# Performance work log

Measured on AMD Instinct MI355X. Metric: run time of the kernel, lower is better.

Reference implementation:

```python
import jax, jax.numpy as jnp
import numpy as np

SCORE_THR = 0.05
IOU_THR = 0.5
TOPK = 1000  # per-class candidate cap (static shape for jit)


def _make_anchors(img):
    """RetinaNet anchors: 9 per location over P3-P7 (strides 8..128)."""
    strides = [8, 16, 32, 64, 128]
    sizes = [32, 64, 128, 256, 512]
    ratios = [0.5, 1.0, 2.0]
    scales = [2.0 ** 0, 2.0 ** (1.0 / 3.0), 2.0 ** (2.0 / 3.0)]
    out = []
    for stride, size in zip(strides, sizes):
        ws, hs = [], []
        for r in ratios:
            for sc in scales:
                a = (size * sc) ** 2
                w = np.sqrt(a / r)
                ws.append(w)
                hs.append(w * r)
        ws = np.asarray(ws)
        hs = np.asarray(hs)
        fs = img // stride
        c = (np.arange(fs) + 0.5) * stride
        cy, cx = np.meshgrid(c, c, indexing='ij')
        cx = cx.reshape(-1)[:, None]
        cy = cy.reshape(-1)[:, None]
        boxes = np.stack([cx - ws / 2, cy - hs / 2, cx + ws / 2, cy + hs / 2], axis=-1)
        out.append(boxes.reshape(-1, 4))
    return np.concatenate(out, axis=0).astype(np.float32)


def setup_inputs() -> dict:
    key = jax.random.key(0)
    k1, k2 = jax.random.split(key)
    img = 1024
    anchors = jnp.asarray(_make_anchors(img))          # [196416, 4]
    A = anchors.shape[0]
    cls_heads = jax.random.uniform(k1, (1, A, 80), dtype=jnp.float32)   # post-sigmoid probs
    reg_heads = jax.random.normal(k2, (1, A, 4), dtype=jnp.float32)
    return {"cls_heads": cls_heads, "reg_heads": reg_heads, "anchors": anchors,
            "img_h": img, "img_w": img}


def _decode(anchors, deltas):
    # BBoxTransform: std = [0.1, 0.1, 0.2, 0.2]
    w = anchors[:, 2] - anchors[:, 0]
    h = anchors[:, 3] - anchors[:, 1]
    cx = anchors[:, 0] + 0.5 * w
    cy = anchors[:, 1] + 0.5 * h
    dx = deltas[:, 0] * 0.1
    dy = deltas[:, 1] * 0.1
    dw = deltas[:, 2] * 0.2
    dh = deltas[:, 3] * 0.2
    pcx = cx + dx * w
    pcy = cy + dy * h
    pw = jnp.exp(dw) * w
    ph = jnp.exp(dh) * h
    return jnp.stack([pcx - 0.5 * pw, pcy - 0.5 * ph,
                      pcx + 0.5 * pw, pcy + 0.5 * ph], axis=-1)


def _iou(b):  # [K,4] -> [K,K]
    area = jnp.maximum(b[:, 2] - b[:, 0], 0) * jnp.maximum(b[:, 3] - b[:, 1], 0)
    lt = jnp.maximum(b[:, None, :2], b[None, :, :2])
    rb = jnp.minimum(b[:, None, 2:], b[None, :, 2:])
    wh = jnp.maximum(rb - lt, 0.0)
    inter = wh[..., 0] * wh[..., 1]
    union = area[:, None] + area[None, :] - inter
    return inter / jnp.maximum(union, 1e-8)


def _nms_one_class(scores_c, boxes):
    # threshold, take top-K candidates (static shape), greedy NMS
    masked = jnp.where(scores_c > SCORE_THR, scores_c, -1.0)
    _, idx = jax.lax.top_k(masked, TOPK)
    s = scores_c[idx]                       # [K]
    b = boxes[idx]                          # [K,4]
    valid = s > SCORE_THR
    iou = _iou(b)                           # [K,K]
    rng = jnp.arange(TOPK)

    def body(i, keep):
        sup = (iou[i] > IOU_THR) & (rng > i) & keep[i]
        return keep & ~sup

    keep = jax.lax.fori_loop(0, TOPK, body, valid)
    return jnp.where(keep, s, 0.0), jnp.where(keep[:, None], b, 0.0), keep


def reference(cls_heads, reg_heads, anchors, img_h, img_w):
    # batch = 1 (the torch code squeezes the batch dim)
    scores_ac = cls_heads[0]                # [A, C]
    deltas = reg_heads[0]                   # [A, 4]
    boxes = _decode(anchors, deltas)        # [A, 4]
    # ClipBoxes
    boxes = jnp.stack([
        jnp.clip(boxes[:, 0], 0.0, img_w),
        jnp.clip(boxes[:, 1], 0.0, img_h),
        jnp.clip(boxes[:, 2], 0.0, img_w),
        jnp.clip(boxes[:, 3], 0.0, img_h)], axis=-1)
    scores_ca = scores_ac.T                 # [C, A]
    s, b, keep = jax.vmap(_nms_one_class, in_axes=(0, None))(scores_ca, boxes)
    C = scores_ca.shape[0]
    cls_idx = jnp.where(keep, jnp.arange(C)[:, None], -1)
    # padded, static-shape equivalent of (finalScores, finalAnchorBoxesIndexes,
    # finalAnchorBoxesCoordinates); invalid slots have score 0 / class -1
    return s.reshape(-1), cls_idx.reshape(-1), b.reshape(-1, 4)
```

## Files before the change

kernel.cpp:

```cpp
#include <hip/hip_runtime.h>
#include <hip/hip_bf16.h>
#include <math.h>

typedef unsigned long long u64;
typedef unsigned int u32;

#define C_NUM 80
#define TOPK 1000
#define CAP 2048
#define HB 128
#define STG 32
#define NCHUNK 16
#define SCORE_THR 0.05f
#define IOU_THR 0.5f
#define GRID_SCAN 256

__device__ __forceinline__ float exp_cr(float x) {
    return (float)exp((double)x);
}

__device__ __forceinline__ void decode_box(const float* __restrict__ anch,
                                           const float* __restrict__ reg,
                                           int a, float fw, float fh, float4* out) {
#pragma clang fp contract(off)
    float a0 = anch[(size_t)a * 4 + 0], a1 = anch[(size_t)a * 4 + 1];
    float a2 = anch[(size_t)a * 4 + 2], a3 = anch[(size_t)a * 4 + 3];
    float d0 = reg[(size_t)a * 4 + 0], d1 = reg[(size_t)a * 4 + 1];
    float d2 = reg[(size_t)a * 4 + 2], d3 = reg[(size_t)a * 4 + 3];
    float w = a2 - a0, h = a3 - a1;
    float cx = a0 + 0.5f * w, cy = a1 + 0.5f * h;
    float dx = d0 * 0.1f, dy = d1 * 0.1f, dw = d2 * 0.2f, dh = d3 * 0.2f;
    float t1 = dx * w; float pcx = cx + t1;
    float t2 = dy * h; float pcy = cy + t2;
    float pw = exp_cr(dw) * w;
    float ph = exp_cr(dh) * h;
    float x1 = pcx - 0.5f * pw, y1 = pcy - 0.5f * ph;
    float x2 = pcx + 0.5f * pw, y2 = pcy + 0.5f * ph;
    x1 = fminf(fmaxf(x1, 0.0f), fw);
    y1 = fminf(fmaxf(y1, 0.0f), fh);
    x2 = fminf(fmaxf(x2, 0.0f), fw);
    y2 = fminf(fmaxf(y2, 0.0f), fh);
    *out = make_float4(x1, y1, x2, y2);
}

__global__ __launch_bounds__(1024)
void hist_kernel(const float4* __restrict__ cls4, u32* __restrict__ slices,
                 u32* __restrict__ cntG, int nvec) {
    __shared__ u32 h[C_NUM * HB];
    int tid = threadIdx.x;
    if (blockIdx.x == 0 && tid < C_NUM) cntG[tid] = 0u;
    for (int i = tid; i < C_NUM * HB; i += 1024) h[i] = 0u;
    __syncthreads();
    int gid = blockIdx.x * 1024 + tid;
    const int stride = GRID_SCAN * 1024;
    const int dC = (stride * 4) % C_NUM;
    int c0 = (gid * 4) % C_NUM;
    for (int v = gid; v < nvec; v += stride) {
        float4 f = cls4[v];
        float e[4] = {f.x, f.y, f.z, f.w};
        int cc = c0;
#pragma unroll
        for (int k = 0; k < 4; ++k) {
            int t = (((int)__float_as_uint(e[k])) - 0x3F000000) >> 16;
            if (t > 0) {
                t = t > HB - 1 ? HB - 1 : t;
                atomicAdd(&h[cc * HB + t], 1u);
            }
            cc++; if (cc == C_NUM) cc = 0;
        }
        c0 += dC; if (c0 >= C_NUM) c0 -= C_NUM;
    }
    __syncthreads();
    u32* my = slices + (size_t)blockIdx.x * (C_NUM * HB);
    for (int i = tid; i < C_NUM * HB; i += 1024) my[i] = h[i];
}

__global__ __launch_bounds__(1024)
void thr_kernel(const u32* __restrict__ slices, u32* __restrict__ thrG) {
    __shared__ u32 part[8][HB];
    __shared__ u32 s[HB];
    __shared__ int bsel;
    int c = blockIdx.x, tid = threadIdx.x;
    int b = tid & (HB - 1), g = tid >> 7;
    u32 sum = 0;
    const u32* base = slices + c * HB + b;
    for (int sl = g * 32; sl < g * 32 + 32; ++sl)
        sum += base[(size_t)sl * (C_NUM * HB)];
    part[g][b] = sum;
    if (tid == 0) bsel = 0;
    __syncthreads();
    if (tid < HB) {
        u32 t = 0;
#pragma unroll
        for (int g2 = 0; g2 < 8; ++g2) t += part[g2][tid];
        s[tid] = t;
    }
    __syncthreads();
    for (int d = 1; d < HB; d <<= 1) {
        u32 v = 0;
        if (tid < HB) v = s[tid] + ((tid + d < HB) ? s[tid + d] : 0u);
        __syncthreads();
        if (tid < HB) s[tid] = v;
        __syncthreads();
    }
    if (tid < HB) {
        u32 me = s[tid];
        u32 nxt = (tid < HB - 1) ? s[tid + 1] : 0u;
        if (me >= (u32)TOPK && (tid == HB - 1 || nxt < (u32)TOPK)) bsel = tid;
    }
    __syncthreads();
    if (tid == 0) {
        int bb = bsel;
        thrG[c] = (bb == 0) ? 0u : (u32)(0x3F000000 + (bb << 16));
    }
}

__global__ __launch_bounds__(1024)
void gather_kernel(const float4* __restrict__ cls4, const u32* __restrict__ thrG,
                   u32* __restrict__ cntG, u64* __restrict__ pool, int nvec) {
    __shared__ int thrS[C_NUM];
    __shared__ u32 lcnt[C_NUM];
    __shared__ u32 lbase[C_NUM];
    __shared__ u64 stage[C_NUM * STG];
    int tid = threadIdx.x;
    if (tid < C_NUM) { thrS[tid] = (int)thrG[tid]; lcnt[tid] = 0u; }
    __syncthreads();

    int gid = blockIdx.x * 1024 + tid;
    const int stride = GRID_SCAN * 1024;
    const int dA = (stride * 4) / C_NUM;
    const int dC = (stride * 4) % C_NUM;
    int base = gid * 4;
    int aa0 = base / C_NUM;
    int c0 = base - aa0 * C_NUM;
    for (int v = gid; v < nvec; v += stride) {
        float4 f = cls4[v];
        float e[4] = {f.x, f.y, f.z, f.w};
        int cc = c0, aa = aa0;
#pragma unroll
        for (int k = 0; k < 4; ++k) {
            int bits = (int)__float_as_uint(e[k]);
            if (bits >= thrS[cc]) {
                u64 key = ((u64)(u32)bits << 32) | (u64)(u32)(~(u32)aa);
                u32 p = atomicAdd(&lcnt[cc], 1u);
                if (p < STG) stage[cc * STG + p] = key;
                else {
                    u32 q = atomicAdd(&cntG[cc], 1u);
                    if (q < CAP) pool[(size_t)cc * CAP + q] = key;
                }
            }
            cc++; if (cc == C_NUM) { cc = 0; aa++; }
        }
        c0 += dC;
        if (c0 >= C_NUM) { c0 -= C_NUM; aa0 += dA + 1; } else aa0 += dA;
    }
    __syncthreads();
    if (tid < C_NUM) {
        u32 nl = lcnt[tid]; if (nl > STG) nl = STG;
        lbase[tid] = nl ? atomicAdd(&cntG[tid], nl) : 0u;
        lcnt[tid] = nl;
    }
    __syncthreads();
    for (int i = tid; i < C_NUM * STG; i += 1024) {
        int c = i >> 5, k = i & (STG - 1);
        if ((u32)k < lcnt[c]) {
            u32 q = lbase[c] + (u32)k;
            if (q < CAP) pool[(size_t)c * CAP + q] = stage[i];
        }
    }
}

__global__ __launch_bounds__(256)
void rank_kernel(const u64* __restrict__ pool, const u32* __restrict__ cntG,
                 const float* __restrict__ anchors, const float* __restrict__ regs,
                 const int* __restrict__ imh, const int* __restrict__ imw,
                 u64* __restrict__ sortedKey, float4* __restrict__ candBox,
                 float* __restrict__ candArea) {
    __shared__ __align__(16) u64 keys[CAP];
    int c = blockIdx.x, q = blockIdx.y, tid = threadIdx.x;
    int n = (int)cntG[c]; if (n > CAP) n = CAP;
    int my = q * 256 + tid;
    if (my >= n && my < TOPK) {
        int g = c * TOPK + my;
        sortedKey[g] = 0ull;
        candBox[g] = make_float4(0.f, 0.f, 0.f, 0.f);
        candArea[g] = 0.f;
    }
    if (q * 256 >= n) return;
    for (int i = tid; i < n; i += 256) keys[i] = pool[(size_t)c * CAP + i];
    __syncthreads();
    u64 k0 = (my < n) ? keys[my] : ~0ull;
    int r0 = 0;
    int j = 0;
    for (; j + 8 <= n; j += 8) {
        ulonglong2 p0 = *(const ulonglong2*)&keys[j];
        ulonglong2 p1 = *(const ulonglong2*)&keys[j + 2];
        ulonglong2 p2 = *(const ulonglong2*)&keys[j + 4];
        ulonglong2 p3 = *(const ulonglong2*)&keys[j + 6];
        r0 += (int)(p0.x > k0) + (int)(p0.y > k0)
            + (int)(p1.x > k0) + (int)(p1.y > k0)
            + (int)(p2.x > k0) + (int)(p2.y > k0)
            + (int)(p3.x > k0) + (int)(p3.y > k0);
    }
    for (; j < n; ++j) r0 += (int)(keys[j] > k0);
    if (my < n && r0 < TOPK) {
        float sc = __uint_as_float((u32)(k0 >> 32));
        int a = (int)(~(u32)k0);
        float fw = (float)(*imw), fh = (float)(*imh);
        float4 bx = make_float4(0.f, 0.f, 0.f, 0.f);
        if (sc > SCORE_THR) decode_box(anchors, regs, a, fw, fh, &bx);
        int g = c * TOPK + r0;
        sortedKey[g] = k0;
        candBox[g] = bx;
        candArea[g] = fmaxf(bx.z - bx.x, 0.0f) * fmaxf(bx.w - bx.y, 0.0f);
    }
}

__global__ __launch_bounds__(512)
void iou_kernel(const float4* __restrict__ candBox, const float* __restrict__ candArea,
                u64* __restrict__ supT) {
#pragma clang fp contract(off)
    __shared__ float4 box[NCHUNK * 64];
    __shared__ float area[NCHUNK * 64];
    int c = blockIdx.x, bq = blockIdx.y;
    int tid = threadIdx.x, lane = tid & 63, wave = tid >> 6;
    for (int i = tid; i < NCHUNK * 64; i += 512) {
        if (i < TOPK) {
            box[i] = candBox[(size_t)c * TOPK + i];
            area[i] = candArea[(size_t)c * TOPK + i];
        } else {
            box[i] = make_float4(0.f, 0.f, 0.f, 0.f);
            area[i] = 0.f;
        }
    }
    __syncthreads();

    int wid = bq * 8 + wave;
    int q = 0, rem = wid;
    while (rem >= ((17 - q) >> 1)) { rem -= (17 - q) >> 1; ++q; }
    int jwA = q + 2 * rem;
    int jwB = jwA + 1;
    bool hasB = (jwB < NCHUNK);
    bool diag = (rem == 0);

    int rowBase = q << 6;
    int jA = (jwA << 6) | lane;
    int jB = hasB ? ((jwB << 6) | lane) : jA;
    float4 bjA = box[jA]; float ajA = area[jA];
    float4 bjB = box[jB]; float ajB = area[jB];
    u64 vwA = 0ull, vwB = 0ull;

#pragma unroll 16
    for (int r = 0; r < 64; ++r) {
        int i = rowBase + r;
        float4 bi = box[i];
        float ai = area[i];
        float ltxA = fmaxf(bi.x, bjA.x), ltyA = fmaxf(bi.y, bjA.y);
        float rbxA = fminf(bi.z, bjA.z), rbyA = fminf(bi.w, bjA.w);
        float wwA = fmaxf(rbxA - ltxA, 0.0f), hhA = fmaxf(rbyA - ltyA, 0.0f);
        float interA = wwA * hhA;
        float dA = fmaxf((ai + ajA) - interA, 1e-8f);
        bool supA = (interA + interA) > dA;
        float ltxB = fmaxf(bi.x, bjB.x), ltyB = fmaxf(bi.y, bjB.y);
        float rbxB = fminf(bi.z, bjB.z), rbyB = fminf(bi.w, bjB.w);
        float wwB = fmaxf(rbxB - ltxB, 0.0f), hhB = fmaxf(rbyB - ltyB, 0.0f);
        float interB = wwB * hhB;
        float dB = fmaxf((ai + ajB) - interB, 1e-8f);
        bool supB = (interB + interB) > dB;

        u64 wA = __ballot(supA);
        u64 wB = __ballot(supB);
        if (diag) wA &= (((~0ull) << 1) << r);
        bool sel = (lane == r);
        vwA = sel ? wA : vwA;
        vwB = sel ? wB : vwB;
    }

    int rowEnd = TOPK - rowBase; if (rowEnd > 64) rowEnd = 64;
    u64* clsBase = supT + (size_t)c * (NCHUNK * 1024);
    if (lane < rowEnd) {
        clsBase[(size_t)jwA * 1024 + rowBase + lane] = vwA;
        if (hasB) clsBase[(size_t)jwB * 1024 + rowBase + lane] = vwB;
    }
}

__global__ __launch_bounds__(1024)
void nmsout_kernel(const u64* __restrict__ supT, const u64* __restrict__ sortedKey,
                   const float4* __restrict__ candBox, float* __restrict__ out) {
    __shared__ __align__(16) u64 supLds[NCHUNK * 1024];
    __shared__ u64 km[NCHUNK];
    __shared__ u64 maskArr[NCHUNK * 64];
    __shared__ int changed;
    int c = blockIdx.x, tid = threadIdx.x;
    int lane = tid & 63, wave = tid >> 6;

    const u64* base = supT + (size_t)c * (NCHUNK * 1024);
#pragma unroll
    for (int jw = 0; jw < NCHUNK; ++jw) {
        int R = (jw + 1) << 6; if (R > TOPK) R = TOPK;
        for (int i = tid; i < R; i += 1024)
            supLds[jw * 1024 + i] = base[(size_t)jw * 1024 + i];
    }

    u64 key = (tid < TOPK) ? sortedKey[c * TOPK + tid] : 0ull;
    float sc = __uint_as_float((u32)(key >> 32));
    bool valid = (tid < TOPK) && (sc > SCORE_THR);
    u64 kwValid = __ballot(valid);
    if (lane == 0) km[wave] = kwValid;
    if (tid == 0) changed = 1;
    __syncthreads();

    while (changed) {
        maskArr[tid] = 0ull - ((km[wave] >> lane) & 1ull);
        __syncthreads();
        if (tid == 0) changed = 0;
        u64 acc = 0ull;
        int R = (wave + 1) << 6;
        for (int i = lane; i < R; i += 64)
            acc |= supLds[wave * 1024 + i] & maskArr[i];
        u32 lo = (u32)acc, hi = (u32)(acc >> 32);
#pragma unroll
        for (int s = 1; s < 64; s <<= 1) {
            lo |= __shfl_xor(lo, s);
            hi |= __shfl_xor(hi, s);
        }
        u64 nk = kwValid & ~(((u64)hi << 32) | lo);
        __syncthreads();
        if (lane == 0) {
            if (nk != km[wave]) changed = 1;
            km[wave] = nk;
        }
        __syncthreads();
    }

    u64 kw = km[wave];
    if (tid < TOPK) {
        bool keep = (kw >> lane) & 1ull;
        int g = c * TOPK + tid;
        out[g] = keep ? sc : 0.0f;
        out[C_NUM * TOPK + g] = keep ? (float)c : -1.0f;
        float4 b = keep ? candBox[(size_t)c * TOPK + tid]
                        : make_float4(0.f, 0.f, 0.f, 0.f);
        ((float4*)(out + 2 * C_NUM * TOPK))[g] = b;
    }
}

extern "C" void kernel_launch(void* const* d_in, const int* in_sizes, int n_in,
                              void* d_out, int out_size, void* d_ws, size_t ws_size,
                              hipStream_t stream) {
    const float* cls  = (const float*)d_in[0];
    const float* reg  = (const float*)d_in[1];
    const float* anch = (const float*)d_in[2];
    const int* imh    = (const int*)d_in[3];
    const int* imw    = (const int*)d_in[4];
    int A = in_sizes[2] / 4;
    int nvec = (A * C_NUM) / 4;

    char* w = (char*)d_ws;
    size_t off = 0;
    auto alloc = [&](size_t bytes) -> void* {
        off = (off + 255) & ~(size_t)255;
        void* p = w + off;
        off += bytes;
        return p;
    };
    u32*    cntG      = (u32*)   alloc((size_t)C_NUM * 4);
    u32*    thrG      = (u32*)   alloc((size_t)C_NUM * 4);
    u32*    slices    = (u32*)   alloc((size_t)GRID_SCAN * C_NUM * HB * 4);
    u64*    pool      = (u64*)   alloc((size_t)C_NUM * CAP * 8);
    u64*    sortedKey = (u64*)   alloc((size_t)C_NUM * TOPK * 8);
    float4* candBox   = (float4*)alloc((size_t)C_NUM * TOPK * 16);
    float*  candArea  = (float*) alloc((size_t)C_NUM * TOPK * 4);
    u64*    supT      = (u64*)   alloc((size_t)C_NUM * NCHUNK * 1024 * 8);

    hist_kernel<<<GRID_SCAN, 1024, 0, stream>>>((const float4*)cls, slices, cntG, nvec);
    thr_kernel<<<C_NUM, 1024, 0, stream>>>(slices, thrG);
    gather_kernel<<<GRID_SCAN, 1024, 0, stream>>>((const float4*)cls, thrG, cntG, pool, nvec);
    rank_kernel<<<dim3(C_NUM, 8), 256, 0, stream>>>(pool, cntG, anch, reg, imh, imw,
                                                    sortedKey, candBox, candArea);
    iou_kernel<<<dim3(C_NUM, 9), 512, 0, stream>>>(candBox, candArea, supT);
    nmsout_kernel<<<C_NUM, 1024, 0, stream>>>(supT, sortedKey, candBox, (float*)d_out);
}
```

Before: 107.1 us.

## Build IoU bitmasks per lane with shift-or instead of ballots; simplify NMS mask loop

The IoU kernel now gives each lane one row box and loops over the 64 column boxes (read as LDS broadcasts), building each suppression word with a shift-or. This replaces the two ballots and lane-select per row, and the diagonal mask is applied once at the end. Blocks shrink to 256 threads and the grid doubles to keep the same wave count. The NMS loop drops the shared maskArr and its extra barrier, reading keep bits straight from km, and each thread's candidate box is loaded before the loop instead of at output time.

```diff
diff --git a/kernel.cpp b/kernel.cpp
--- a/kernel.cpp
+++ b/kernel.cpp
@@ -216,7 +216,7 @@
     }
 }
 
-__global__ __launch_bounds__(512)
+__global__ __launch_bounds__(256)
 void iou_kernel(const float4* __restrict__ candBox, const float* __restrict__ candArea,
                 u64* __restrict__ supT) {
 #pragma clang fp contract(off)
@@ -224,7 +224,7 @@
     __shared__ float area[NCHUNK * 64];
     int c = blockIdx.x, bq = blockIdx.y;
     int tid = threadIdx.x, lane = tid & 63, wave = tid >> 6;
-    for (int i = tid; i < NCHUNK * 64; i += 512) {
+    for (int i = tid; i < NCHUNK * 64; i += 256) {
         if (i < TOPK) {
             box[i] = candBox[(size_t)c * TOPK + i];
             area[i] = candArea[(size_t)c * TOPK + i];
@@ -235,47 +235,44 @@
     }
     __syncthreads();
 
-    int wid = bq * 8 + wave;
+    int wid = bq * 4 + wave;
     int q = 0, rem = wid;
     while (rem >= ((17 - q) >> 1)) { rem -= (17 - q) >> 1; ++q; }
     int jwA = q + 2 * rem;
     int jwB = jwA + 1;
     bool hasB = (jwB < NCHUNK);
-    bool diag = (rem == 0);
 
     int rowBase = q << 6;
-    int jA = (jwA << 6) | lane;
-    int jB = hasB ? ((jwB << 6) | lane) : jA;
-    float4 bjA = box[jA]; float ajA = area[jA];
-    float4 bjB = box[jB]; float ajB = area[jB];
+    int i = rowBase + lane;
+    float4 bi = box[i];
+    float ai = area[i];
+    int jbA = jwA << 6;
+    int jbB = hasB ? (jwB << 6) : jbA;
     u64 vwA = 0ull, vwB = 0ull;
 
 #pragma unroll 16
-    for (int r = 0; r < 64; ++r) {
-        int i = rowBase + r;
-        float4 bi = box[i];
-        float ai = area[i];
+    for (int jj = 63; jj >= 0; --jj) {
+        float4 bjA = box[jbA + jj]; float ajA = area[jbA + jj];
         float ltxA = fmaxf(bi.x, bjA.x), ltyA = fmaxf(bi.y, bjA.y);
         float rbxA = fminf(bi.z, bjA.z), rbyA = fminf(bi.w, bjA.w);
         float wwA = fmaxf(rbxA - ltxA, 0.0f), hhA = fmaxf(rbyA - ltyA, 0.0f);
         float interA = wwA * hhA;
         float dA = fmaxf((ai + ajA) - interA, 1e-8f);
-        bool supA = (interA + interA) > dA;
+        u64 supA = (u64)((interA + interA) > dA);
+
+        float4 bjB = box[jbB + jj]; float ajB = area[jbB + jj];
         float ltxB = fmaxf(bi.x, bjB.x), ltyB = fmaxf(bi.y, bjB.y);
         float rbxB = fminf(bi.z, bjB.z), rbyB = fminf(bi.w, bjB.w);
         float wwB = fmaxf(rbxB - ltxB, 0.0f), hhB = fmaxf(rbyB - ltyB, 0.0f);
         float interB = wwB * hhB;
         float dB = fmaxf((ai + ajB) - interB, 1e-8f);
-        bool supB = (interB + interB) > dB;
-
-        u64 wA = __ballot(supA);
-        u64 wB = __ballot(supB);
-        if (diag) wA &= (((~0ull) << 1) << r);
-        bool sel = (lane == r);
-        vwA = sel ? wA : vwA;
-        vwB = sel ? wB : vwB;
-    }
-
+        u64 supB = (u64)((interB + interB) > dB);
+
+        vwA = (vwA << 1) | supA;
+        vwB = (vwB << 1) | supB;
+    }
+
+    if (jwA == q) vwA &= ((~0ull) << 1) << lane;
     int rowEnd = TOPK - rowBase; if (rowEnd > 64) rowEnd = 64;
     u64* clsBase = supT + (size_t)c * (NCHUNK * 1024);
     if (lane < rowEnd) {
@@ -289,7 +286,6 @@
                    const float4* __restrict__ candBox, float* __restrict__ out) {
     __shared__ __align__(16) u64 supLds[NCHUNK * 1024];
     __shared__ u64 km[NCHUNK];
-    __shared__ u64 maskArr[NCHUNK * 64];
     __shared__ int changed;
     int c = blockIdx.x, tid = threadIdx.x;
     int lane = tid & 63, wave = tid >> 6;
@@ -304,6 +300,8 @@
 
     u64 key = (tid < TOPK) ? sortedKey[c * TOPK + tid] : 0ull;
     float sc = __uint_as_float((u32)(key >> 32));
+    float4 bx = (tid < TOPK) ? candBox[(size_t)c * TOPK + tid]
+                             : make_float4(0.f, 0.f, 0.f, 0.f);
     bool valid = (tid < TOPK) && (sc > SCORE_THR);
     u64 kwValid = __ballot(valid);
     if (lane == 0) km[wave] = kwValid;
@@ -311,13 +309,12 @@
     __syncthreads();
 
     while (changed) {
-        maskArr[tid] = 0ull - ((km[wave] >> lane) & 1ull);
-        __syncthreads();
-        if (tid == 0) changed = 0;
         u64 acc = 0ull;
         int R = (wave + 1) << 6;
-        for (int i = lane; i < R; i += 64)
-            acc |= supLds[wave * 1024 + i] & maskArr[i];
+        for (int i = lane; i < R; i += 64) {
+            u64 kword = km[i >> 6];
+            acc |= supLds[wave * 1024 + i] & (0ull - ((kword >> (i & 63)) & 1ull));
+        }
         u32 lo = (u32)acc, hi = (u32)(acc >> 32);
 #pragma unroll
         for (int s = 1; s < 64; s <<= 1) {
@@ -325,6 +322,8 @@
             hi |= __shfl_xor(hi, s);
         }
         u64 nk = kwValid & ~(((u64)hi << 32) | lo);
+        __syncthreads();
+        if (tid == 0) changed = 0;
         __syncthreads();
         if (lane == 0) {
             if (nk != km[wave]) changed = 1;
@@ -339,8 +338,7 @@
         int g = c * TOPK + tid;
         out[g] = keep ? sc : 0.0f;
         out[C_NUM * TOPK + g] = keep ? (float)c : -1.0f;
-        float4 b = keep ? candBox[(size_t)c * TOPK + tid]
-                        : make_float4(0.f, 0.f, 0.f, 0.f);
+        float4 b = keep ? bx : make_float4(0.f, 0.f, 0.f, 0.f);
         ((float4*)(out + 2 * C_NUM * TOPK))[g] = b;
     }
 }
@@ -378,6 +376,6 @@
     gather_kernel<<<GRID_SCAN, 1024, 0, stream>>>((const float4*)cls, thrG, cntG, pool, nvec);
     rank_kernel<<<dim3(C_NUM, 8), 256, 0, stream>>>(pool, cntG, anch, reg, imh, imw,
                                                     sortedKey, candBox, candArea);
-    iou_kernel<<<dim3(C_NUM, 9), 512, 0, stream>>>(candBox, candArea, supT);
+    iou_kernel<<<dim3(C_NUM, 18), 256, 0, stream>>>(candBox, candArea, supT);
     nmsout_kernel<<<C_NUM, 1024, 0, stream>>>(supT, sortedKey, candBox, (float*)d_out);
 }
```

After: 112.8 us. 5.3% more time.

## Fuse IoU suppression-matrix kernel into NMS kernel via shared memory

Applied to the files above, without the earlier changes.

Merges the IoU bitmask computation and the iterative NMS resolution into one kernel per class, so the suppression matrix is built directly in LDS instead of being written to and read back from global memory. This removes one launch and the global round-trip of the suppression matrix, and reuses the LDS boxes for output. In exchange, IoU work per class drops from 9 blocks to a single 1024-thread block (80 blocks total), which lowers parallelism across the GPU's compute units.

```diff
diff --git a/kernel.cpp b/kernel.cpp
--- a/kernel.cpp
+++ b/kernel.cpp
@@ -216,98 +216,77 @@
     }
 }
 
-__global__ __launch_bounds__(512)
-void iou_kernel(const float4* __restrict__ candBox, const float* __restrict__ candArea,
-                u64* __restrict__ supT) {
+__global__ __launch_bounds__(1024, 1)
+void iounms_kernel(const float4* __restrict__ candBox, const float* __restrict__ candArea,
+                   const u64* __restrict__ sortedKey, float* __restrict__ out) {
 #pragma clang fp contract(off)
+    __shared__ __align__(16) u64 supLds[NCHUNK * 1024];
     __shared__ float4 box[NCHUNK * 64];
     __shared__ float area[NCHUNK * 64];
-    int c = blockIdx.x, bq = blockIdx.y;
-    int tid = threadIdx.x, lane = tid & 63, wave = tid >> 6;
-    for (int i = tid; i < NCHUNK * 64; i += 512) {
-        if (i < TOPK) {
-            box[i] = candBox[(size_t)c * TOPK + i];
-            area[i] = candArea[(size_t)c * TOPK + i];
-        } else {
-            box[i] = make_float4(0.f, 0.f, 0.f, 0.f);
-            area[i] = 0.f;
-        }
-    }
-    __syncthreads();
-
-    int wid = bq * 8 + wave;
-    int q = 0, rem = wid;
-    while (rem >= ((17 - q) >> 1)) { rem -= (17 - q) >> 1; ++q; }
-    int jwA = q + 2 * rem;
-    int jwB = jwA + 1;
-    bool hasB = (jwB < NCHUNK);
-    bool diag = (rem == 0);
-
-    int rowBase = q << 6;
-    int jA = (jwA << 6) | lane;
-    int jB = hasB ? ((jwB << 6) | lane) : jA;
-    float4 bjA = box[jA]; float ajA = area[jA];
-    float4 bjB = box[jB]; float ajB = area[jB];
-    u64 vwA = 0ull, vwB = 0ull;
-
-#pragma unroll 16
-    for (int r = 0; r < 64; ++r) {
-        int i = rowBase + r;
-        float4 bi = box[i];
-        float ai = area[i];
-        float ltxA = fmaxf(bi.x, bjA.x), ltyA = fmaxf(bi.y, bjA.y);
-        float rbxA = fminf(bi.z, bjA.z), rbyA = fminf(bi.w, bjA.w);
-        float wwA = fmaxf(rbxA - ltxA, 0.0f), hhA = fmaxf(rbyA - ltyA, 0.0f);
-        float interA = wwA * hhA;
-        float dA = fmaxf((ai + ajA) - interA, 1e-8f);
-        bool supA = (interA + interA) > dA;
-        float ltxB = fmaxf(bi.x, bjB.x), ltyB = fmaxf(bi.y, bjB.y);
-        float rbxB = fminf(bi.z, bjB.z), rbyB = fminf(bi.w, bjB.w);
-        float wwB = fmaxf(rbxB - ltxB, 0.0f), hhB = fmaxf(rbyB - ltyB, 0.0f);
-        float interB = wwB * hhB;
-        float dB = fmaxf((ai + ajB) - interB, 1e-8f);
-        bool supB = (interB + interB) > dB;
-
-        u64 wA = __ballot(supA);
-        u64 wB = __ballot(supB);
-        if (diag) wA &= (((~0ull) << 1) << r);
-        bool sel = (lane == r);
-        vwA = sel ? wA : vwA;
-        vwB = sel ? wB : vwB;
-    }
-
-    int rowEnd = TOPK - rowBase; if (rowEnd > 64) rowEnd = 64;
-    u64* clsBase = supT + (size_t)c * (NCHUNK * 1024);
-    if (lane < rowEnd) {
-        clsBase[(size_t)jwA * 1024 + rowBase + lane] = vwA;
-        if (hasB) clsBase[(size_t)jwB * 1024 + rowBase + lane] = vwB;
-    }
-}
-
-__global__ __launch_bounds__(1024)
-void nmsout_kernel(const u64* __restrict__ supT, const u64* __restrict__ sortedKey,
-                   const float4* __restrict__ candBox, float* __restrict__ out) {
-    __shared__ __align__(16) u64 supLds[NCHUNK * 1024];
     __shared__ u64 km[NCHUNK];
     __shared__ u64 maskArr[NCHUNK * 64];
     __shared__ int changed;
     int c = blockIdx.x, tid = threadIdx.x;
     int lane = tid & 63, wave = tid >> 6;
 
-    const u64* base = supT + (size_t)c * (NCHUNK * 1024);
-#pragma unroll
-    for (int jw = 0; jw < NCHUNK; ++jw) {
-        int R = (jw + 1) << 6; if (R > TOPK) R = TOPK;
-        for (int i = tid; i < R; i += 1024)
-            supLds[jw * 1024 + i] = base[(size_t)jw * 1024 + i];
-    }
-
+    if (tid < TOPK) {
+        box[tid] = candBox[(size_t)c * TOPK + tid];
+        area[tid] = candArea[(size_t)c * TOPK + tid];
+    } else {
+        box[tid] = make_float4(0.f, 0.f, 0.f, 0.f);
+        area[tid] = 0.f;
+    }
     u64 key = (tid < TOPK) ? sortedKey[c * TOPK + tid] : 0ull;
     float sc = __uint_as_float((u32)(key >> 32));
     bool valid = (tid < TOPK) && (sc > SCORE_THR);
     u64 kwValid = __ballot(valid);
     if (lane == 0) km[wave] = kwValid;
     if (tid == 0) changed = 1;
+    __syncthreads();
+
+    for (int dt = wave; dt < 72; dt += NCHUNK) {
+        int q = 0, rem = dt;
+        while (rem >= ((17 - q) >> 1)) { rem -= (17 - q) >> 1; ++q; }
+        int jwA = q + 2 * rem;
+        int jwB = jwA + 1;
+        bool hasB = (jwB < NCHUNK);
+        bool diag = (rem == 0);
+
+        int rowBase = q << 6;
+        int jA = (jwA << 6) | lane;
+        int jB = hasB ? ((jwB << 6) | lane) : jA;
+        float4 bjA = box[jA]; float ajA = area[jA];
+        float4 bjB = box[jB]; float ajB = area[jB];
+        u64 vwA = 0ull, vwB = 0ull;
+
+#pragma unroll 16
+        for (int r = 0; r < 64; ++r) {
+            int i = rowBase + r;
+            float4 bi = box[i];
+            float ai = area[i];
+            float ltxA = fmaxf(bi.x, bjA.x), ltyA = fmaxf(bi.y, bjA.y);
+            float rbxA = fminf(bi.z, bjA.z), rbyA = fminf(bi.w, bjA.w);
+            float wwA = fmaxf(rbxA - ltxA, 0.0f), hhA = fmaxf(rbyA - ltyA, 0.0f);
+            float interA = wwA * hhA;
+            float dA = fmaxf((ai + ajA) - interA, 1e-8f);
+            bool supA = (interA + interA) > dA;
+            float ltxB = fmaxf(bi.x, bjB.x), ltyB = fmaxf(bi.y, bjB.y);
+            float rbxB = fminf(bi.z, bjB.z), rbyB = fminf(bi.w, bjB.w);
+            float wwB = fmaxf(rbxB - ltxB, 0.0f), hhB = fmaxf(rbyB - ltyB, 0.0f);
+            float interB = wwB * hhB;
+            float dB = fmaxf((ai + ajB) - interB, 1e-8f);
+            bool supB = (interB + interB) > dB;
+
+            u64 wA = __ballot(supA);
+            u64 wB = __ballot(supB);
+            if (diag) wA &= (((~0ull) << 1) << r);
+            bool sel = (lane == r);
+            vwA = sel ? wA : vwA;
+            vwB = sel ? wB : vwB;
+        }
+        supLds[jwA * 1024 + rowBase + lane] = vwA;
+        if (hasB) supLds[jwB * 1024 + rowBase + lane] = vwB;
+    }
     __syncthreads();
 
     while (changed) {
@@ -339,8 +318,7 @@
         int g = c * TOPK + tid;
         out[g] = keep ? sc : 0.0f;
         out[C_NUM * TOPK + g] = keep ? (float)c : -1.0f;
-        float4 b = keep ? candBox[(size_t)c * TOPK + tid]
-                        : make_float4(0.f, 0.f, 0.f, 0.f);
+        float4 b = keep ? box[tid] : make_float4(0.f, 0.f, 0.f, 0.f);
         ((float4*)(out + 2 * C_NUM * TOPK))[g] = b;
     }
 }
@@ -371,13 +349,11 @@
     u64*    sortedKey = (u64*)   alloc((size_t)C_NUM * TOPK * 8);
     float4* candBox   = (float4*)alloc((size_t)C_NUM * TOPK * 16);
     float*  candArea  = (float*) alloc((size_t)C_NUM * TOPK * 4);
-    u64*    supT      = (u64*)   alloc((size_t)C_NUM * NCHUNK * 1024 * 8);
 
     hist_kernel<<<GRID_SCAN, 1024, 0, stream>>>((const float4*)cls, slices, cntG, nvec);
     thr_kernel<<<C_NUM, 1024, 0, stream>>>(slices, thrG);
     gather_kernel<<<GRID_SCAN, 1024, 0, stream>>>((const float4*)cls, thrG, cntG, pool, nvec);
     rank_kernel<<<dim3(C_NUM, 8), 256, 0, stream>>>(pool, cntG, anch, reg, imh, imw,
                                                     sortedKey, candBox, candArea);
-    iou_kernel<<<dim3(C_NUM, 9), 512, 0, stream>>>(candBox, candArea, supT);
-    nmsout_kernel<<<C_NUM, 1024, 0, stream>>>(supT, sortedKey, candBox, (float*)d_out);
-}
+    iounms_kernel<<<C_NUM, 1024, 0, stream>>>(candBox, candArea, sortedKey, (float*)d_out);
+}
```

Measured after the change: 149.4 us. 1.4x slower.
